# Performance work log

Measured on AMD Instinct MI355X. Metric: run time of the kernel, lower is better.

Reference implementation:

```python
import jax, jax.numpy as jnp
import numpy as np

N = 8192   # total points (all batches)
B = 2      # batch size
PC_MIN = jnp.array([-50.0, -50.0, -5.0], dtype=jnp.float32)
PC_EXT = jnp.array([100.0, 100.0, 8.0], dtype=jnp.float32)
VOXEL = jnp.array([0.3, 0.3, 6.0], dtype=jnp.float32)
GX, GY, GZ = 334, 334, 2   # grid dims = ceil(extent / voxel)
CONNECTED_DIST = 0.6       # cfg_per_class['Car']['connected_dist']
MIN_POINTS = 1             # cfg_per_class['Car']['min_points']


def setup_inputs() -> dict:
    key = jax.random.key(0)
    k1, k2 = jax.random.split(key)
    points = jax.random.uniform(k1, (N, 3), dtype=jnp.float32) * PC_EXT + PC_MIN
    batch_idx = jax.random.randint(k2, (N,), 0, B, dtype=jnp.int32)
    return {"points": points, "batch_idx": batch_idx}


def _voxel_centers_per_point(points, batch_idx):
    # coors = floor((p - pc_range[:3]) / voxel_size)  (scatter_v2 'avg' over (b,z,y,x))
    coors = jnp.floor((points - PC_MIN) / VOXEL).astype(jnp.int32)
    cx = jnp.clip(coors[:, 0], 0, GX - 1)
    cy = jnp.clip(coors[:, 1], 0, GY - 1)
    cz = jnp.clip(coors[:, 2], 0, GZ - 1)
    vid = ((batch_idx * GZ + cz) * GY + cy) * GX + cx  # linear voxel id, fixed grid
    NV = B * GZ * GY * GX
    ones = jnp.ones((points.shape[0],), dtype=jnp.float32)
    cnt = jax.ops.segment_sum(ones, vid, num_segments=NV)          # [NV]
    sums = jax.ops.segment_sum(points, vid, num_segments=NV)        # [NV,3]
    centers = sums / jnp.maximum(cnt, 1.0)[:, None]                  # voxel means
    return centers[vid], cnt[vid]  # gathered back per point (== cluster_inds[inv_inds] pattern)


def reference(points, batch_idx):
    cpp, cnt_pp = _voxel_centers_per_point(points, batch_idx)
    # filter_almost_empty: points whose voxel holds >= min_points
    valid = cnt_pp >= MIN_POINTS
    n = points.shape[0]
    # find_connected_components: xy pairwise distance between voxel centers,
    # computed per-point (points sharing a voxel share a center -> dist 0 ->
    # identical components as the voxel-level CC in the original).
    d = cpp[:, None, :2] - cpp[None, :, :2]          # [N,N,2]
    dist = jnp.sqrt(jnp.sum(d * d, axis=-1))         # [N,N]
    same_b = batch_idx[:, None] == batch_idx[None, :]
    vv = valid[:, None] & valid[None, :]
    adj = ((dist < CONNECTED_DIST) & same_b & vv) | jnp.eye(n, dtype=bool)
    # connected components via min-label propagation to fixed point
    labels0 = jnp.arange(n, dtype=jnp.int32)

    def cond(carry):
        return carry[1]

    def body(carry):
        lab, _ = carry
        new = jnp.min(jnp.where(adj, lab[None, :], n), axis=1).astype(jnp.int32)
        return (new, jnp.any(new != lab))

    labels, _ = jax.lax.while_loop(cond, body, (labels0, jnp.array(True)))
    # canonical component id = min point index in component (invalid points -> -1)
    cluster = jnp.where(valid, labels, -1)
    cluster_inds = jnp.stack([batch_idx, cluster], axis=1)  # [batch, cluster_id]
    return cluster_inds, valid, cpp
```

## Files before the change

kernel.cpp:

```cpp
#include <hip/hip_runtime.h>

#define NPTS  8192
#define GXD   334
#define GYD   334
#define GZD   2
#define BATCH 2
#define NV    (BATCH * GZD * GYD * GXD)
#define NVP   446464
#define KADJ  50

#define GBLK  512
#define GTHR  1024

__device__ __forceinline__ int rep_find(int* parent, int v) {
    int curr = parent[v];
    if (curr != v) {
        int prev = v, next;
        while (curr > (next = parent[curr])) {
            parent[prev] = next;
            prev = curr;
            curr = next;
        }
    }
    return curr;
}

__device__ __forceinline__ void unite(int* parent, int u, int v) {
    int ru = rep_find(parent, u);
    int rv = rep_find(parent, v);
    while (ru != rv) {
        if (ru < rv) { int t = ru; ru = rv; rv = t; }
        int prev = atomicCAS(&parent[ru], ru, rv);
        if (prev == ru) return;
        ru = rep_find(parent, prev);
        rv = rep_find(parent, rv);
    }
}

__global__ void k_accum(const float* __restrict__ pts, const int* __restrict__ bidx,
                        float* cnt, float* sx, float* sy, float* sz, int* rep,
                        int* parent, int* pvid) {
    int i = blockIdx.x * blockDim.x + threadIdx.x;
    if (i >= NPTS) return;
    parent[i] = i;
    float x = pts[3 * i + 0], y = pts[3 * i + 1], z = pts[3 * i + 2];
    int cx = (int)floorf((x - (-50.0f)) / 0.3f);
    int cy = (int)floorf((y - (-50.0f)) / 0.3f);
    int cz = (int)floorf((z - (-5.0f))  / 6.0f);
    cx = min(max(cx, 0), GXD - 1);
    cy = min(max(cy, 0), GYD - 1);
    cz = min(max(cz, 0), GZD - 1);
    int b = bidx[i];
    pvid[i] = cx | (cy << 9) | (cz << 18) | (b << 19);
    int vid = ((b * GZD + cz) * GYD + cy) * GXD + cx;
    atomicAdd(&cnt[vid], 1.0f);
    atomicAdd(&sx[vid], x);
    atomicAdd(&sy[vid], y);
    atomicAdd(&sz[vid], z);
    atomicMax(&rep[vid], NPTS - i);
}

__global__ void __launch_bounds__(GTHR) k_gather(
        const int* __restrict__ pvid,
        const float* __restrict__ cnt, const float* __restrict__ sx,
        const float* __restrict__ sy, const float* __restrict__ sz,
        const int* __restrict__ rep,
        int* parent, int* done, float* __restrict__ out) {
    int tid  = blockIdx.x * GTHR + threadIdx.x;
    int i    = tid >> 6;
    int lane = tid & 63;

    int p  = pvid[i];
    int cx = p & 511, cy = (p >> 9) & 511, cz = (p >> 18) & 1, b = (p >> 19) & 1;
    int vid = ((b * GZD + cz) * GYD + cy) * GXD + cx;

    bool  occ = false;
    float ncn = 1.0f, nxc = 0.0f, nyc = 0.0f;
    int   nrep = 0;
    if (lane < KADJ) {
        int zz  = lane / 25;
        int rem = lane % 25;
        int dy  = rem / 5 - 2;
        int dx  = rem % 5 - 2;
        int ny = cy + dy, nx = cx + dx;
        if (ny >= 0 && ny < GYD && nx >= 0 && nx < GXD) {
            int nvid = ((b * GZD + zz) * GYD + ny) * GXD + nx;
            float c = cnt[nvid];
            if (c > 0.0f) {
                occ  = true;
                ncn  = fmaxf(c, 1.0f);
                nxc  = sx[nvid] / ncn;
                nyc  = sy[nvid] / ncn;
                nrep = NPTS - rep[nvid];
            }
        }
    }

    int lane_own = cz * 25 + 12;
    float cxf    = __shfl(nxc, lane_own);
    float cyf    = __shfl(nyc, lane_own);
    float cn_own = __shfl(ncn, lane_own);

    if (occ) {
        float ddx = cxf - nxc;
        float ddy = cyf - nyc;
        float sq = __fadd_rn(__fmul_rn(ddx, ddx), __fmul_rn(ddy, ddy));
        if (sqrtf(sq) < 0.6f && nrep != i)
            unite(parent, i, nrep);
    }

    if (lane == 0) {
        out[2 * i]                = (float)b;
        out[2 * NPTS + i]         = 1.0f;
        out[3 * NPTS + 3 * i + 0] = cxf;
        out[3 * NPTS + 3 * i + 1] = cyf;
        out[3 * NPTS + 3 * i + 2] = sz[vid] / cn_own;
    }

    __shared__ int l[NPTS];
    __shared__ int isLast;
    __syncthreads();
    if (threadIdx.x == 0)
        isLast = (atomicAdd(done, 1) == GBLK - 1);
    __syncthreads();
    if (!isLast) return;

    for (int j = threadIdx.x; j < NPTS; j += GTHR)
        l[j] = __hip_atomic_load(&parent[j], __ATOMIC_RELAXED, __HIP_MEMORY_SCOPE_AGENT);
    __syncthreads();

    for (int j = threadIdx.x; j < NPTS; j += GTHR) {
        int r = l[j];
        for (;;) {
            int rr = l[r];
            if (rr == r) break;
            r = rr;
        }
        out[2 * j + 1] = (float)r;
    }
}

extern "C" void kernel_launch(void* const* d_in, const int* in_sizes, int n_in,
                              void* d_out, int out_size, void* d_ws, size_t ws_size,
                              hipStream_t stream) {
    const float* pts  = (const float*)d_in[0];
    const int*   bidx = (const int*)d_in[1];
    float* out = (float*)d_out;

    char* w = (char*)d_ws;
    float* cnt    = (float*)(w + 0L * NVP * 4);
    float* sx     = (float*)(w + 1L * NVP * 4);
    float* sy     = (float*)(w + 2L * NVP * 4);
    float* sz     = (float*)(w + 3L * NVP * 4);
    int*   rep    = (int*)  (w + 4L * NVP * 4);
    int*   done   = (int*)  (w + 4L * NVP * 4 + NVP * 4 - 256);
    int*   parent = (int*)  (w + 5L * NVP * 4);
    int*   pvid   = (int*)  (w + 5L * NVP * 4 + 32768);

    hipMemsetAsync(w, 0, 5L * NVP * 4, stream);

    hipLaunchKernelGGL(k_accum, dim3(NPTS / 256), dim3(256), 0, stream,
                       pts, bidx, cnt, sx, sy, sz, rep, parent, pvid);
    hipLaunchKernelGGL(k_gather, dim3(GBLK), dim3(GTHR), 0, stream,
                       pvid, cnt, sx, sy, sz, rep, parent, done, out);
}
```

Measured before the change: 29.27 us.

## Shrink gather blocks and drop 32KB shared label copy in final pass

Changes the gather kernel to 2048 blocks of 256 threads, still one wavefront per point. It removes the 32KB shared-memory copy of the parent array, which limited how many blocks fit per CU. The last block now resolves roots by pointer-chasing in global memory, 16 independent chains per thread in two passes, iterating until no chain changes. This should raise occupancy for the neighbour-gather phase. In exchange, the serial tail runs on only 256 threads with global-memory latency per hop instead of LDS.

```diff
diff --git a/kernel.cpp b/kernel.cpp
--- a/kernel.cpp
+++ b/kernel.cpp
@@ -9,8 +9,9 @@
 #define NVP   446464
 #define KADJ  50
 
-#define GBLK  512
-#define GTHR  1024
+#define GBLK  2048
+#define GTHR  256
+#define TGRP  16
 
 __device__ __forceinline__ int rep_find(int* parent, int v) {
     int curr = parent[v];
@@ -117,7 +118,6 @@
         out[3 * NPTS + 3 * i + 2] = sz[vid] / cn_own;
     }
 
-    __shared__ int l[NPTS];
     __shared__ int isLast;
     __syncthreads();
     if (threadIdx.x == 0)
@@ -125,18 +125,28 @@
     __syncthreads();
     if (!isLast) return;
 
-    for (int j = threadIdx.x; j < NPTS; j += GTHR)
-        l[j] = __hip_atomic_load(&parent[j], __ATOMIC_RELAXED, __HIP_MEMORY_SCOPE_AGENT);
-    __syncthreads();
-
-    for (int j = threadIdx.x; j < NPTS; j += GTHR) {
-        int r = l[j];
-        for (;;) {
-            int rr = l[r];
-            if (rr == r) break;
-            r = rr;
+    for (int pass = 0; pass < 2; pass++) {
+        int base = pass * (GTHR * TGRP) + threadIdx.x;
+        int r[TGRP];
+#pragma unroll
+        for (int k = 0; k < TGRP; k++)
+            r[k] = __hip_atomic_load(&parent[base + k * GTHR],
+                                     __ATOMIC_RELAXED, __HIP_MEMORY_SCOPE_AGENT);
+        bool changed = true;
+        while (changed) {
+            changed = false;
+            int nr[TGRP];
+#pragma unroll
+            for (int k = 0; k < TGRP; k++)
+                nr[k] = __hip_atomic_load(&parent[r[k]],
+                                          __ATOMIC_RELAXED, __HIP_MEMORY_SCOPE_AGENT);
+#pragma unroll
+            for (int k = 0; k < TGRP; k++)
+                if (nr[k] != r[k]) { r[k] = nr[k]; changed = true; }
         }
-        out[2 * j + 1] = (float)r;
+#pragma unroll
+        for (int k = 0; k < TGRP; k++)
+            out[2 * (base + k * GTHR) + 1] = (float)r[k];
     }
 }
 
@@ -153,7 +163,7 @@
     float* sy     = (float*)(w + 2L * NVP * 4);
     float* sz     = (float*)(w + 3L * NVP * 4);
     int*   rep    = (int*)  (w + 4L * NVP * 4);
-    int*   done   = (int*)  (w + 4L * NVP * 4 + NVP * 4 - 256);
+    int*   done   = (int*)  (w + 5L * NVP * 4 - 256);
     int*   parent = (int*)  (w + 5L * NVP * 4);
     int*   pvid   = (int*)  (w + 5L * NVP * 4 + 32768);
 
```

Measured after the change: 46.62 us. 1.59x slower.
